# Optimization experiments

Hardware: AMD Instinct MI355X
Metric: run time of the kernel (lower is better)

The kernel has to match this reference:

```python
import jax, jax.numpy as jnp
import numpy as np

# Multi-res hash grid config (tiny-cuda-nn defaults matching input_ch=32 = 16 levels * 2 feats)
L = 16            # n_levels
F = 2             # n_features_per_level
T = 2 ** 19       # hashmap size per level
BASE_RES = 16
FINEST_RES = 512
_b = np.exp((np.log(FINEST_RES) - np.log(BASE_RES)) / (L - 1))
RES = np.floor(BASE_RES * (_b ** np.arange(L))).astype(np.float32)  # (L,)
PRIMES = jnp.array([1, 2654435761, 805459861], dtype=jnp.uint32)
# 8 binary corner offsets of a voxel
CORNERS = jnp.array([[(i >> d) & 1 for d in range(3)] for i in range(8)], dtype=jnp.uint32)  # (8,3)


def hash_encode(x, tables):
    """x: (N,3) in [0,1]; tables: (L, T, F). Returns (N, L*F)."""
    res = jnp.asarray(RES)                              # (L,)
    xs = x[None, :, :] * res[:, None, None]             # (L,N,3) scaled coords
    x0f = jnp.floor(xs)
    frac = xs - x0f                                     # (L,N,3)
    x0 = x0f.astype(jnp.uint32)
    corners = x0[:, :, None, :] + CORNERS[None, None]   # (L,N,8,3) uint32
    # spatial hash: xor of coord*prime, wraparound uint32 mul
    h = (corners[..., 0] * PRIMES[0]) ^ (corners[..., 1] * PRIMES[1]) ^ (corners[..., 2] * PRIMES[2])
    idx = (h % jnp.uint32(T)).astype(jnp.int32)         # (L,N,8)
    gidx = idx + (jnp.arange(L, dtype=jnp.int32) * T)[:, None, None]
    feats = tables.reshape(L * T, F)[gidx]              # (L,N,8,F) gather
    # trilinear weights per corner
    w = jnp.prod(jnp.where(CORNERS[None, None] == 1, frac[:, :, None, :], 1.0 - frac[:, :, None, :]), axis=-1)  # (L,N,8)
    out = jnp.einsum('lnc,lncf->lnf', w, feats)         # (L,N,F)
    return out.transpose(1, 0, 2).reshape(x.shape[0], L * F)


def setup_inputs() -> dict:
    key = jax.random.key(0)
    ks = jax.random.split(key, 16)
    N = 1048576
    W = 128
    pos_flat = jax.random.uniform(ks[0], (N, 3), dtype=jnp.float32)  # world pts in unit cube
    bbox_min = jnp.zeros((3,), dtype=jnp.float32)
    bbox_max = jnp.ones((3,), dtype=jnp.float32)
    tables = jax.random.uniform(ks[1], (L, T, F), dtype=jnp.float32, minval=-1e-4, maxval=1e-4)
    def lin(k, fan_in, fan_out):
        s = 1.0 / np.sqrt(fan_in)
        return jax.random.uniform(k, (fan_in, fan_out), dtype=jnp.float32, minval=-s, maxval=s)
    return {
        'pos_flat': pos_flat, 'bbox_min': bbox_min, 'bbox_max': bbox_max, 'tables': tables,
        'W0': lin(ks[2], L * F, W), 'b0': jnp.zeros((W,), jnp.float32),
        'W1': lin(ks[3], W, W), 'b1': jnp.zeros((W,), jnp.float32),
        'W2': lin(ks[4], W, W), 'b2': jnp.zeros((W,), jnp.float32),
        'W3': lin(ks[5], W, W), 'b3': jnp.zeros((W,), jnp.float32),
        'Wout': lin(ks[6], W, 4), 'bout': jnp.zeros((4,), jnp.float32),
    }


def reference(pos_flat, bbox_min, bbox_max, tables, W0, b0, W1, b1, W2, b2, W3, b3, Wout, bout):
    # normalize into canonical bbox [0,1]^3
    x = (pos_flat - bbox_min) / (bbox_max - bbox_min)
    h = hash_encode(x, tables)                # (N, 32)
    h = jax.nn.relu(h @ W0 + b0)
    h = jax.nn.relu(h @ W1 + b1)
    h = jax.nn.relu(h @ W2 + b2)
    h = jax.nn.relu(h @ W3 + b3)
    raws = h @ Wout + bout                    # (N, 4) rgb + density
    return raws
```

## Files before the change

kernel.cpp:

```cpp
#include <hip/hip_runtime.h>

typedef _Float16 half8 __attribute__((ext_vector_type(8)));
typedef _Float16 half4 __attribute__((ext_vector_type(4)));
typedef _Float16 half2 __attribute__((ext_vector_type(2)));
typedef float    f32x4 __attribute__((ext_vector_type(4)));
typedef float    f32x2 __attribute__((ext_vector_type(2)));
typedef unsigned u32x2 __attribute__((ext_vector_type(2)));
typedef unsigned u32x4 __attribute__((ext_vector_type(4)));

#define TMASK ((1u << 19) - 1u)
#define HSTRIDE 136
constexpr float SCALE = 65536.0f;
constexpr float INV_SCALE = 1.0f / 65536.0f;

__device__ __constant__ unsigned SC_TAB[8]   = {18, 22, 27, 34, 42, 52, 66, 82};
__device__ __constant__ unsigned SX4_TAB[8]  = {5, 6, 7, 9, 11, 13, 17, 21};
__device__ __constant__ unsigned DOFF16_TAB[8] = {0, 1620, 4524, 9627, 20031, 39435, 74587, 148639};
#define DSLOT_TOTAL 289843u

__global__ void prep_kernel(const float* __restrict__ W0, const float* __restrict__ W1,
                            const float* __restrict__ W2, const float* __restrict__ W3,
                            const float* __restrict__ Wm,
                            const float* __restrict__ b0, const float* __restrict__ b1,
                            const float* __restrict__ b2, const float* __restrict__ b3,
                            const float* __restrict__ bm,
                            _Float16* __restrict__ wsW, float* __restrict__ wsB,
                            const float* __restrict__ tabSrc, _Float16* __restrict__ tabF,
                            int tabBlocks)
{
    if ((int)blockIdx.x < tabBlocks) {
        size_t i = (size_t)blockIdx.x * 256 + threadIdx.x;
        f32x4 v = ((const f32x4*)tabSrc)[i];
        half4 o;
        o[0] = (_Float16)(v.x * SCALE);
        o[1] = (_Float16)(v.y * SCALE);
        o[2] = (_Float16)(v.z * SCALE);
        o[3] = (_Float16)(v.w * SCALE);
        ((half4*)tabF)[i] = o;
        return;
    }
    int gid = ((int)blockIdx.x - tabBlocks) * 256 + threadIdx.x;
    if (gid < 6912) {
        int tile = gid >> 6, lane = gid & 63;
        const float* W; int K, N, toff;
        if (tile < 8)        { W = W0; K = 32;  N = 128; toff = 0;   }
        else if (tile < 40)  { W = W1; K = 128; N = 128; toff = 8;   }
        else if (tile < 72)  { W = W2; K = 128; N = 128; toff = 40;  }
        else if (tile < 104) { W = W3; K = 128; N = 128; toff = 72;  }
        else                 { W = Wm; K = 128; N = 4;   toff = 104; }
        int tt = tile - toff;
        int KT = K >> 5;
        int nt = tt / KT, kt = tt - nt * KT;
        int n = nt * 16 + (lane & 15);
        int kbase = kt * 32 + (lane >> 4) * 8;
        half8 v;
        #pragma unroll
        for (int j = 0; j < 8; j++) {
            int k = kbase + j;
            float w = (n < N) ? W[k * N + n] : 0.0f;
            v[j] = (_Float16)w;
        }
        *(half8*)(wsW + (size_t)gid * 8) = v;
    } else if (gid < 6912 + 528) {
        int i = gid - 6912;
        float v;
        if (i < 512) {
            int layer = i >> 7, n = i & 127;
            const float* b = (layer == 0) ? b0 : (layer == 1) ? b1 : (layer == 2) ? b2 : b3;
            v = b[n] * SCALE;
        } else {
            int n = i - 512;
            v = (n < 4) ? bm[n] * SCALE : 0.0f;
        }
        wsB[i] = v;
    }
}

__global__ void dense_build(const float* __restrict__ tables, unsigned* __restrict__ dense)
{
    unsigned e = blockIdx.x * 256 + threadIdx.x;
    if (e >= DSLOT_TOTAL * 4u) return;
    unsigned slot = e >> 2, j = e & 3u;
    int l = 0;
    #pragma unroll
    for (int i = 1; i < 8; i++) l += (slot >= DOFF16_TAB[i]) ? 1 : 0;
    unsigned local = slot - DOFF16_TAB[l];
    unsigned s = SC_TAB[l], sx4 = SX4_TAB[l];
    unsigned plane = sx4 * s;
    unsigned z = local / plane;
    unsigned rem = local - z * plane;
    unsigned y = rem / sx4;
    unsigned xs = rem - y * sx4;
    unsigned x = xs * 4u + j;
    unsigned h = (x ^ (y * 2654435761u) ^ (z * 805459861u)) & TMASK;
    const float* src = tables + ((size_t)l * 524288u + h) * 2;
    half2 o; o[0] = (_Float16)(src[0] * SCALE); o[1] = (_Float16)(src[1] * SCALE);
    union { half2 h2; unsigned u; } cv; cv.h2 = o;
    dense[e] = cv.u;
}

__global__ __launch_bounds__(256, 4) void encode_kernel(
    const float* __restrict__ pos, const float* __restrict__ bmn, const float* __restrict__ bmx,
    const _Float16* __restrict__ tabFine, const u32x4* __restrict__ dense16,
    _Float16* __restrict__ feat, int npts)
{
    const int lvl0 = (int)(blockIdx.x & 7);
    const int t = (int)threadIdx.x;
    const long p0 = (long)(blockIdx.x >> 3) * 512 + t;
    const float bx = bmn[0], by = bmn[1], bz = bmn[2];
    const float dxr = bmx[0] - bx, dyr = bmx[1] - by, dzr = bmx[2] - bz;
    constexpr float RESL[16] = {16.f, 20.f, 25.f, 32.f, 40.f, 50.f, 64.f, 80.f,
                                101.f, 128.f, 161.f, 203.f, 256.f, 322.f, 406.f, 512.f};
    const int l1 = lvl0 + 8;
    const _Float16* tblB = tabFine + ((size_t)lvl0 << 20);
    const float resF = RESL[l1], resC = RESL[lvl0];
    const unsigned s   = SC_TAB[lvl0];
    const unsigned sx4 = SX4_TAB[lvl0];
    const unsigned plane = sx4 * s;
    const u32x4* dptr = dense16 + DOFF16_TAB[lvl0];

    unsigned fSlot[2][4], fOdd[2][4], cBase[2][4];
    unsigned peM[2], kC[2];
    bool oddF[2], nx3[2];
    float fF[2][3], fC[2][3];

    #pragma unroll
    for (int pt = 0; pt < 2; pt++) {
        const long p = p0 + pt * 256;
        const float nx = (pos[p * 3 + 0] - bx) / dxr;
        const float ny = (pos[p * 3 + 1] - by) / dyr;
        const float nz = (pos[p * 3 + 2] - bz) / dzr;
        {
            float xs = nx * resF, ys = ny * resF, zs = nz * resF;
            float fx = floorf(xs), fy = floorf(ys), fz = floorf(zs);
            unsigned xi = (unsigned)fx, yi = (unsigned)fy, zi = (unsigned)fz;
            fF[pt][0] = xs - fx; fF[pt][1] = ys - fy; fF[pt][2] = zs - fz;
            unsigned hy0 = yi * 2654435761u, hy1 = (yi + 1u) * 2654435761u;
            unsigned hz0 = zi * 805459861u,  hz1 = (zi + 1u) * 805459861u;
            unsigned hyz[4] = {hy0 ^ hz0, hy1 ^ hz0, hy0 ^ hz1, hy1 ^ hz1};
            unsigned e = (xi + 1u) & ~1u, o = xi | 1u;
            oddF[pt] = (xi & 1u) != 0u;
            unsigned m = 0;
            #pragma unroll
            for (int g = 0; g < 4; g++) {
                unsigned ie = (e ^ hyz[g]) & TMASK;
                fSlot[pt][g] = ie & ~1u;
                m |= (ie & 1u) << g;
                fOdd[pt][g] = (o ^ hyz[g]) & TMASK;
            }
            peM[pt] = m;
        }
        {
            float xs = nx * resC, ys = ny * resC, zs = nz * resC;
            float fx = floorf(xs), fy = floorf(ys), fz = floorf(zs);
            unsigned xi = (unsigned)fx, yi = (unsigned)fy, zi = (unsigned)fz;
            fC[pt][0] = xs - fx; fC[pt][1] = ys - fy; fC[pt][2] = zs - fz;
            unsigned b00 = (xi >> 2) + sx4 * yi + plane * zi;
            cBase[pt][0] = b00;
            cBase[pt][1] = b00 + sx4;
            cBase[pt][2] = b00 + plane;
            cBase[pt][3] = b00 + plane + sx4;
            kC[pt] = xi & 3u;
            nx3[pt] = (kC[pt] == 3u);
        }
    }

    u32x2 fS[2][4]; u32x4 cS[2][4]; unsigned fO[2][4], cN[2][4];
    #pragma unroll
    for (int pt = 0; pt < 2; pt++) {
        #pragma unroll
        for (int g = 0; g < 4; g++)
            fS[pt][g] = *(const u32x2*)(tblB + (size_t)fSlot[pt][g] * 2);
        #pragma unroll
        for (int g = 0; g < 4; g++)
            cS[pt][g] = dptr[cBase[pt][g]];
        if (oddF[pt]) {
            #pragma unroll
            for (int g = 0; g < 4; g++)
                fO[pt][g] = *(const unsigned*)(tblB + (size_t)fOdd[pt][g] * 2);
        }
        if (nx3[pt]) {
            #pragma unroll
            for (int g = 0; g < 4; g++)
                cN[pt][g] = *(const unsigned*)(dptr + cBase[pt][g] + 1);
        }
    }

    #pragma unroll
    for (int pt = 0; pt < 2; pt++) {
        const long p = p0 + pt * 256;
        {
            float tx = fF[pt][0], ty = fF[pt][1], tz = fF[pt][2];
            float wyz[4] = {(1.0f - ty) * (1.0f - tz), ty * (1.0f - tz),
                            (1.0f - ty) * tz,          ty * tz};
            float b0 = 0.0f, b1 = 0.0f;
            #pragma unroll
            for (int g = 0; g < 4; g++) {
                union { unsigned u; half2 h; } lo, hi, ov;
                lo.u = fS[pt][g][0]; hi.u = fS[pt][g][1];
                bool pe = ((peM[pt] >> g) & 1u) != 0u;
                half2 fe  = pe ? hi.h : lo.h;
                half2 fe1 = pe ? lo.h : hi.h;
                ov.u = oddF[pt] ? fO[pt][g] : 0u;
                half2 fx0 = oddF[pt] ? ov.h : fe;
                half2 fx1 = oddF[pt] ? fe : fe1;
                float w0 = wyz[g] * (1.0f - tx), w1 = wyz[g] * tx;
                b0 += w0 * (float)fx0[0] + w1 * (float)fx1[0];
                b1 += w0 * (float)fx0[1] + w1 * (float)fx1[1];
            }
            half2 ov2; ov2[0] = (_Float16)b0; ov2[1] = (_Float16)b1;
            union { half2 h; unsigned u; } cv; cv.h = ov2;
            __builtin_nontemporal_store(cv.u, (unsigned*)(feat + ((size_t)l1 * npts + p) * 2));
        }
        {
            float tx = fC[pt][0], ty = fC[pt][1], tz = fC[pt][2];
            float wyz[4] = {(1.0f - ty) * (1.0f - tz), ty * (1.0f - tz),
                            (1.0f - ty) * tz,          ty * tz};
            unsigned k = kC[pt];
            unsigned kp1 = (k < 3u) ? (k + 1u) : 0u;
            float a0 = 0.0f, a1 = 0.0f;
            #pragma unroll
            for (int g = 0; g < 4; g++) {
                union { unsigned u; half2 h; } u0, u1;
                u0.u = cS[pt][g][k];
                u1.u = nx3[pt] ? cN[pt][g] : cS[pt][g][kp1];
                float w0 = wyz[g] * (1.0f - tx), w1 = wyz[g] * tx;
                a0 += w0 * (float)u0.h[0] + w1 * (float)u1.h[0];
                a1 += w0 * (float)u0.h[1] + w1 * (float)u1.h[1];
            }
            half2 ov2; ov2[0] = (_Float16)a0; ov2[1] = (_Float16)a1;
            union { half2 h; unsigned u; } cv; cv.h = ov2;
            __builtin_nontemporal_store(cv.u, (unsigned*)(feat + ((size_t)lvl0 * npts + p) * 2));
        }
    }
}

#define ELANE 68

template<int KT, int TOFF>
__device__ __forceinline__ void layer_fwd4(half8 b[4][4], const half8* __restrict__ wf,
                                           const float* __restrict__ wsB, int li,
                                           unsigned* __restrict__ eb, int lane, int quad,
                                           unsigned srcA, unsigned srcB, int mtbase)
{
    unsigned* wptr = eb + lane * ELANE;
    #pragma unroll
    for (int mt = 0; mt < 8; mt++) {
        f32x4 bias = *(const f32x4*)&wsB[li * 128 + mt * 16 + quad * 4];
        half8 w[KT];
        #pragma unroll
        for (int kt = 0; kt < KT; kt++)
            w[kt] = wf[(size_t)(TOFF + mt * KT + kt) * 64 + lane];
        f32x4 acc[4] = {bias, bias, bias, bias};
        #pragma unroll
        for (int nt = 0; nt < 4; nt++)
            #pragma unroll
            for (int kt = 0; kt < KT; kt++)
                acc[nt] = __builtin_amdgcn_mfma_f32_16x16x32_f16(w[kt], b[nt][kt], acc[nt], 0, 0, 0);
        #pragma unroll
        for (int np = 0; np < 2; np++) {
            union { _Float16 h[8]; u32x4 v; } pk;
            #pragma unroll
            for (int r = 0; r < 4; r++) {
                pk.h[r]     = (_Float16)fmaxf(acc[2 * np][r],     0.0f);
                pk.h[4 + r] = (_Float16)fmaxf(acc[2 * np + 1][r], 0.0f);
            }
            *(u32x4*)(wptr + mt * 8 + np * 4) = pk.v;
        }
    }
    #pragma unroll
    for (int ktp = 0; ktp < 4; ktp++) {
        int mt = 2 * ktp + mtbase;
        u32x4 rA0 = *(const u32x4*)(eb + srcA * ELANE + mt * 8);
        u32x4 rA1 = *(const u32x4*)(eb + srcA * ELANE + mt * 8 + 4);
        u32x4 rB0 = *(const u32x4*)(eb + srcB * ELANE + mt * 8);
        u32x4 rB1 = *(const u32x4*)(eb + srcB * ELANE + mt * 8 + 4);
        union { u32x4 v; half8 h; } c0, c1, c2, c3;
        c0.v = (u32x4){rA0[0], rA0[1], rB0[0], rB0[1]};
        c1.v = (u32x4){rA0[2], rA0[3], rB0[2], rB0[3]};
        c2.v = (u32x4){rA1[0], rA1[1], rB1[0], rB1[1]};
        c3.v = (u32x4){rA1[2], rA1[3], rB1[2], rB1[3]};
        b[0][ktp] = c0.h;
        b[1][ktp] = c1.h;
        b[2][ktp] = c2.h;
        b[3][ktp] = c3.h;
    }
}

__global__ __launch_bounds__(256) void mlp_kernel(
    const unsigned* __restrict__ feat32, const half8* __restrict__ wf,
    const float* __restrict__ wsB, float* __restrict__ out, int npts)
{
    __shared__ __align__(16) unsigned ebuf[4 * 64 * ELANE];
    const int t = threadIdx.x;
    const int lane = t & 63, wv = t >> 6;
    const int col = lane & 15, quad = lane >> 4;
    const long base = (long)blockIdx.x * 256 + wv * 64;
    unsigned* eb = ebuf + wv * (64 * ELANE);
    const int q1 = 2 * (quad & 1);
    const unsigned srcA = (unsigned)(col + 16 * q1);
    const unsigned srcB = (unsigned)(col + 16 * (q1 + 1));
    const int mtbase = quad >> 1;

    half8 b[4][4];
    #pragma unroll
    for (int nt = 0; nt < 4; nt++) {
        const long pt = base + nt * 16 + col;
        union { unsigned u4[4]; half8 v; } cv;
        #pragma unroll
        for (int jj = 0; jj < 4; jj++)
            cv.u4[jj] = feat32[(size_t)(quad * 4 + jj) * npts + pt];
        b[nt][0] = cv.v;
    }

    layer_fwd4<1, 0 >(b, wf, wsB, 0, eb, lane, quad, srcA, srcB, mtbase);
    layer_fwd4<4, 8 >(b, wf, wsB, 1, eb, lane, quad, srcA, srcB, mtbase);
    layer_fwd4<4, 40>(b, wf, wsB, 2, eb, lane, quad, srcA, srcB, mtbase);
    layer_fwd4<4, 72>(b, wf, wsB, 3, eb, lane, quad, srcA, srcB, mtbase);

    f32x4 biaso = *(const f32x4*)&wsB[512 + quad * 4];
    f32x4 acco[4] = {biaso, biaso, biaso, biaso};
    #pragma unroll
    for (int kt = 0; kt < 4; kt++) {
        half8 w = wf[(size_t)(104 + kt) * 64 + lane];
        #pragma unroll
        for (int nt = 0; nt < 4; nt++)
            acco[nt] = __builtin_amdgcn_mfma_f32_16x16x32_f16(w, b[nt][kt], acco[nt], 0, 0, 0);
    }
    if (quad == 0) {
        #pragma unroll
        for (int nt = 0; nt < 4; nt++) {
            f32x4 v;
            #pragma unroll
            for (int r = 0; r < 4; r++) v[r] = acco[nt][r] * INV_SCALE;
            *(f32x4*)(out + (base + nt * 16 + col) * 4) = v;
        }
    }
}

template<int KT, int TOFF, bool RELU>
__device__ __forceinline__ void mlp_layer(_Float16* h, const half8* __restrict__ wf,
                                          const float* __restrict__ wsB, int layerIdx,
                                          int m0, int lane)
{
    const int col = lane & 15, quad = lane >> 4;
    const int sw = (col & 3) << 3;
    half8 a[2][KT];
    #pragma unroll
    for (int mt = 0; mt < 2; mt++)
        #pragma unroll
        for (int kt = 0; kt < KT; kt++)
            a[mt][kt] = *(const half8*)&h[(m0 + mt * 16 + col) * HSTRIDE + ((kt * 32 + quad * 8) ^ sw)];
    f32x4 acc[2][8];
    #pragma unroll
    for (int nt = 0; nt < 8; nt++) {
        float bv = wsB[layerIdx * 128 + nt * 16 + col];
        acc[0][nt] = (f32x4){bv, bv, bv, bv};
        acc[1][nt] = (f32x4){bv, bv, bv, bv};
    }
    #pragma unroll
    for (int nt = 0; nt < 8; nt++) {
        half8 b[KT];
        #pragma unroll
        for (int kt = 0; kt < KT; kt++)
            b[kt] = wf[(size_t)(TOFF + nt * KT + kt) * 64 + lane];
        #pragma unroll
        for (int mt = 0; mt < 2; mt++)
            #pragma unroll
            for (int kt = 0; kt < KT; kt++)
                acc[mt][nt] = __builtin_amdgcn_mfma_f32_16x16x32_f16(a[mt][kt], b[kt], acc[mt][nt], 0, 0, 0);
    }
    #pragma unroll
    for (int mt = 0; mt < 2; mt++)
        #pragma unroll
        for (int nt = 0; nt < 8; nt++) {
            f32x4 v = acc[mt][nt];
            #pragma unroll
            for (int r = 0; r < 4; r++) {
                float x = v[r];
                if (RELU) x = fmaxf(x, 0.0f);
                h[(m0 + mt * 16 + quad * 4 + r) * HSTRIDE + ((nt * 16 + col) ^ (r << 3))] = (_Float16)x;
            }
        }
}

__global__ __launch_bounds__(256, 2) void fused_kernel(
    const float* __restrict__ pos, const float* __restrict__ bmn, const float* __restrict__ bmx,
    const float* __restrict__ tables, const half8* __restrict__ wf, const float* __restrict__ wsB,
    float* __restrict__ out)
{
    __shared__ _Float16 hbuf[128 * HSTRIDE];
    __shared__ float outstage[512];
    const int t = threadIdx.x;
    const long base = (long)blockIdx.x * 128;
    {
        const int p = t >> 1, hh = t & 1;
        const long gp = base + p;
        const float b0x = bmn[0], b0y = bmn[1], b0z = bmn[2];
        const float nx = (pos[gp * 3 + 0] - b0x) / (bmx[0] - b0x);
        const float ny = (pos[gp * 3 + 1] - b0y) / (bmx[1] - b0y);
        const float nz = (pos[gp * 3 + 2] - b0z) / (bmx[2] - b0z);
        constexpr float RLO[8] = {16.f, 20.f, 25.f, 32.f, 40.f, 50.f, 64.f, 80.f};
        constexpr float RHI[8] = {101.f, 128.f, 161.f, 203.f, 256.f, 322.f, 406.f, 512.f};
        half8 fa, fb;
        #pragma unroll
        for (int li = 0; li < 8; li++) {
            const float res = hh ? RHI[li] : RLO[li];
            const float* tbl = tables + ((size_t)(hh * 8 + li) << 20);
            float xs = nx * res, ys = ny * res, zs = nz * res;
            float fx = floorf(xs), fy = floorf(ys), fz = floorf(zs);
            unsigned xi = (unsigned)fx, yi = (unsigned)fy, zi = (unsigned)fz;
            float tx = xs - fx, ty = ys - fy, tz = zs - fz;
            unsigned hx[2] = {xi, xi + 1u};
            unsigned hy[2] = {yi * 2654435761u, (yi + 1u) * 2654435761u};
            unsigned hz[2] = {zi * 805459861u, (zi + 1u) * 805459861u};
            float wx[2] = {1.0f - tx, tx}, wy[2] = {1.0f - ty, ty}, wz[2] = {1.0f - tz, tz};
            float a0 = 0.0f, a1 = 0.0f;
            #pragma unroll
            for (int c = 0; c < 8; c++) {
                unsigned hsh = hx[c & 1] ^ hy[(c >> 1) & 1] ^ hz[c >> 2];
                unsigned idx = hsh & TMASK;
                f32x2 f = *(const f32x2*)(tbl + (size_t)idx * 2);
                float w = wx[c & 1] * wy[(c >> 1) & 1] * wz[c >> 2];
                a0 += w * f.x;
                a1 += w * f.y;
            }
            if (li < 4) { fa[2 * li]       = (_Float16)(a0 * SCALE); fa[2 * li + 1]       = (_Float16)(a1 * SCALE); }
            else        { fb[2 * (li - 4)] = (_Float16)(a0 * SCALE); fb[2 * (li - 4) + 1] = (_Float16)(a1 * SCALE); }
        }
        const int sw = (p & 3) << 3;
        *(half8*)&hbuf[p * HSTRIDE + ((hh * 16) ^ sw)]       = fa;
        *(half8*)&hbuf[p * HSTRIDE + (((hh * 16) + 8) ^ sw)] = fb;
    }
    __syncthreads();
    {
        const int lane = t & 63;
        const int m0 = (t >> 6) * 32;
        mlp_layer<1, 0,   true>(hbuf, wf, wsB, 0, m0, lane);
        mlp_layer<4, 8,   true>(hbuf, wf, wsB, 1, m0, lane);
        mlp_layer<4, 40,  true>(hbuf, wf, wsB, 2, m0, lane);
        mlp_layer<4, 72,  true>(hbuf, wf, wsB, 3, m0, lane);
        const int col = lane & 15, quad = lane >> 4;
        const int sw = (col & 3) << 3;
        half8 a[2][4];
        #pragma unroll
        for (int mt = 0; mt < 2; mt++)
            #pragma unroll
            for (int kt = 0; kt < 4; kt++)
                a[mt][kt] = *(const half8*)&hbuf[(m0 + mt * 16 + col) * HSTRIDE + ((kt * 32 + quad * 8) ^ sw)];
        float bv = wsB[512 + col];
        f32x4 acc[2] = {(f32x4){bv, bv, bv, bv}, (f32x4){bv, bv, bv, bv}};
        #pragma unroll
        for (int kt = 0; kt < 4; kt++) {
            half8 bfr = wf[(size_t)(104 + kt) * 64 + lane];
            #pragma unroll
            for (int mt = 0; mt < 2; mt++)
                acc[mt] = __builtin_amdgcn_mfma_f32_16x16x32_f16(a[mt][kt], bfr, acc[mt], 0, 0, 0);
        }
        if (col < 4) {
            #pragma unroll
            for (int mt = 0; mt < 2; mt++)
                #pragma unroll
                for (int r = 0; r < 4; r++)
                    outstage[(m0 + mt * 16 + quad * 4 + r) * 4 + col] = acc[mt][r] * INV_SCALE;
        }
    }
    __syncthreads();
    if (t < 128) {
        f32x4 v = ((const f32x4*)outstage)[t];
        *(f32x4*)(out + (base + t) * 4) = v;
    }
}

extern "C" void kernel_launch(void* const* d_in, const int* in_sizes, int n_in,
                              void* d_out, int out_size, void* d_ws, size_t ws_size,
                              hipStream_t stream) {
    const float* pos    = (const float*)d_in[0];
    const float* bmn    = (const float*)d_in[1];
    const float* bmx    = (const float*)d_in[2];
    const float* tables = (const float*)d_in[3];
    const float* W0 = (const float*)d_in[4];
    const float* b0 = (const float*)d_in[5];
    const float* W1 = (const float*)d_in[6];
    const float* b1 = (const float*)d_in[7];
    const float* W2 = (const float*)d_in[8];
    const float* b2 = (const float*)d_in[9];
    const float* W3 = (const float*)d_in[10];
    const float* b3 = (const float*)d_in[11];
    const float* Wm = (const float*)d_in[12];
    const float* bm = (const float*)d_in[13];

    const int N = in_sizes[0] / 3;
    const size_t featBytes    = (size_t)N * 16 * 4;
    const size_t tabFineBytes = (size_t)8 * 524288 * 2 * 2;
    const size_t denseBytes   = ((size_t)DSLOT_TOTAL * 16 + 255) & ~(size_t)255;
    const size_t need = featBytes + tabFineBytes + denseBytes + 110592 + 2112;

    if (ws_size >= need && (N % 512) == 0) {
        _Float16* feat  = (_Float16*)d_ws;
        _Float16* tabF  = (_Float16*)((char*)d_ws + featBytes);
        unsigned* dense = (unsigned*)((char*)d_ws + featBytes + tabFineBytes);
        _Float16* wsW   = (_Float16*)((char*)d_ws + featBytes + tabFineBytes + denseBytes);
        float*    wsB   = (float*)((char*)d_ws + featBytes + tabFineBytes + denseBytes + 110592);
        prep_kernel<<<8192 + 30, 256, 0, stream>>>(W0, W1, W2, W3, Wm, b0, b1, b2, b3, bm,
                                                   wsW, wsB, tables + (size_t)8 * 524288 * 2,
                                                   tabF, 8192);
        dense_build<<<(DSLOT_TOTAL * 4 + 255) / 256, 256, 0, stream>>>(tables, dense);
        encode_kernel<<<(N / 512) * 8, 256, 0, stream>>>(pos, bmn, bmx, tabF,
                                                         (const u32x4*)dense, feat, N);
        mlp_kernel<<<N / 256, 256, 0, stream>>>((const unsigned*)feat, (const half8*)wsW,
                                                wsB, (float*)d_out, N);
    } else {
        _Float16* wsW = (_Float16*)d_ws;
        float*    wsB = (float*)((char*)d_ws + 110592);
        prep_kernel<<<30, 256, 0, stream>>>(W0, W1, W2, W3, Wm, b0, b1, b2, b3, bm,
                                            wsW, wsB, tables, (_Float16*)nullptr, 0);
        fused_kernel<<<N / 128, 256, 0, stream>>>(pos, bmn, bmx, tables,
                                                  (const half8*)wsW, wsB, (float*)d_out);
    }
}
```

Measured before the change: 617.6 us.

## Software-pipeline encode kernel over eight points per thread with double-buffered loads

The encode kernel now handles eight points per thread instead of two. It uses a two-slot rotation: the gathers for the next point are issued before the current point's loaded values are consumed. The aim is to keep more hash-table gathers in flight per thread and to amortize per-block setup, hiding gather latency. The grid shrinks by four times and the fast path now requires N divisible by 2048. Register pressure may rise and fewer blocks may be in flight.

```diff
diff --git a/kernel.cpp b/kernel.cpp
--- a/kernel.cpp
+++ b/kernel.cpp
@@ -99,6 +99,16 @@
     dense[e] = cv.u;
 }
 
+struct PtState {
+    unsigned fSlot[4], fOdd[4], cBase[4];
+    unsigned peM, kC;
+    bool oddF, nx3;
+    float fF[3], fC[3];
+};
+struct PtLoads {
+    u32x2 fS[4]; u32x4 cS[4]; unsigned fO[4], cN[4];
+};
+
 __global__ __launch_bounds__(256, 4) void encode_kernel(
     const float* __restrict__ pos, const float* __restrict__ bmn, const float* __restrict__ bmx,
     const _Float16* __restrict__ tabFine, const u32x4* __restrict__ dense16,
@@ -106,7 +116,7 @@
 {
     const int lvl0 = (int)(blockIdx.x & 7);
     const int t = (int)threadIdx.x;
-    const long p0 = (long)(blockIdx.x >> 3) * 512 + t;
+    const long pb = (long)(blockIdx.x >> 3) * 2048 + t;
     const float bx = bmn[0], by = bmn[1], bz = bmn[2];
     const float dxr = bmx[0] - bx, dyr = bmx[1] - by, dzr = bmx[2] - bz;
     constexpr float RESL[16] = {16.f, 20.f, 25.f, 32.f, 40.f, 50.f, 64.f, 80.f,
@@ -114,19 +124,11 @@
     const int l1 = lvl0 + 8;
     const _Float16* tblB = tabFine + ((size_t)lvl0 << 20);
     const float resF = RESL[l1], resC = RESL[lvl0];
-    const unsigned s   = SC_TAB[lvl0];
     const unsigned sx4 = SX4_TAB[lvl0];
-    const unsigned plane = sx4 * s;
+    const unsigned plane = sx4 * SC_TAB[lvl0];
     const u32x4* dptr = dense16 + DOFF16_TAB[lvl0];
 
-    unsigned fSlot[2][4], fOdd[2][4], cBase[2][4];
-    unsigned peM[2], kC[2];
-    bool oddF[2], nx3[2];
-    float fF[2][3], fC[2][3];
-
-    #pragma unroll
-    for (int pt = 0; pt < 2; pt++) {
-        const long p = p0 + pt * 256;
+    auto computePt = [&](long p, PtState& S) {
         const float nx = (pos[p * 3 + 0] - bx) / dxr;
         const float ny = (pos[p * 3 + 1] - by) / dyr;
         const float nz = (pos[p * 3 + 2] - bz) / dzr;
@@ -134,76 +136,72 @@
             float xs = nx * resF, ys = ny * resF, zs = nz * resF;
             float fx = floorf(xs), fy = floorf(ys), fz = floorf(zs);
             unsigned xi = (unsigned)fx, yi = (unsigned)fy, zi = (unsigned)fz;
-            fF[pt][0] = xs - fx; fF[pt][1] = ys - fy; fF[pt][2] = zs - fz;
+            S.fF[0] = xs - fx; S.fF[1] = ys - fy; S.fF[2] = zs - fz;
             unsigned hy0 = yi * 2654435761u, hy1 = (yi + 1u) * 2654435761u;
             unsigned hz0 = zi * 805459861u,  hz1 = (zi + 1u) * 805459861u;
             unsigned hyz[4] = {hy0 ^ hz0, hy1 ^ hz0, hy0 ^ hz1, hy1 ^ hz1};
             unsigned e = (xi + 1u) & ~1u, o = xi | 1u;
-            oddF[pt] = (xi & 1u) != 0u;
+            S.oddF = (xi & 1u) != 0u;
             unsigned m = 0;
             #pragma unroll
             for (int g = 0; g < 4; g++) {
                 unsigned ie = (e ^ hyz[g]) & TMASK;
-                fSlot[pt][g] = ie & ~1u;
+                S.fSlot[g] = ie & ~1u;
                 m |= (ie & 1u) << g;
-                fOdd[pt][g] = (o ^ hyz[g]) & TMASK;
+                S.fOdd[g] = (o ^ hyz[g]) & TMASK;
             }
-            peM[pt] = m;
+            S.peM = m;
         }
         {
             float xs = nx * resC, ys = ny * resC, zs = nz * resC;
             float fx = floorf(xs), fy = floorf(ys), fz = floorf(zs);
             unsigned xi = (unsigned)fx, yi = (unsigned)fy, zi = (unsigned)fz;
-            fC[pt][0] = xs - fx; fC[pt][1] = ys - fy; fC[pt][2] = zs - fz;
+            S.fC[0] = xs - fx; S.fC[1] = ys - fy; S.fC[2] = zs - fz;
             unsigned b00 = (xi >> 2) + sx4 * yi + plane * zi;
-            cBase[pt][0] = b00;
-            cBase[pt][1] = b00 + sx4;
-            cBase[pt][2] = b00 + plane;
-            cBase[pt][3] = b00 + plane + sx4;
-            kC[pt] = xi & 3u;
-            nx3[pt] = (kC[pt] == 3u);
-        }
-    }
-
-    u32x2 fS[2][4]; u32x4 cS[2][4]; unsigned fO[2][4], cN[2][4];
-    #pragma unroll
-    for (int pt = 0; pt < 2; pt++) {
+            S.cBase[0] = b00;
+            S.cBase[1] = b00 + sx4;
+            S.cBase[2] = b00 + plane;
+            S.cBase[3] = b00 + plane + sx4;
+            S.kC = xi & 3u;
+            S.nx3 = (S.kC == 3u);
+        }
+    };
+
+    auto issuePt = [&](const PtState& S, PtLoads& L) {
         #pragma unroll
         for (int g = 0; g < 4; g++)
-            fS[pt][g] = *(const u32x2*)(tblB + (size_t)fSlot[pt][g] * 2);
+            L.fS[g] = *(const u32x2*)(tblB + (size_t)S.fSlot[g] * 2);
         #pragma unroll
         for (int g = 0; g < 4; g++)
-            cS[pt][g] = dptr[cBase[pt][g]];
-        if (oddF[pt]) {
+            L.cS[g] = dptr[S.cBase[g]];
+        if (S.oddF) {
             #pragma unroll
             for (int g = 0; g < 4; g++)
-                fO[pt][g] = *(const unsigned*)(tblB + (size_t)fOdd[pt][g] * 2);
-        }
-        if (nx3[pt]) {
+                L.fO[g] = *(const unsigned*)(tblB + (size_t)S.fOdd[g] * 2);
+        }
+        if (S.nx3) {
             #pragma unroll
             for (int g = 0; g < 4; g++)
-                cN[pt][g] = *(const unsigned*)(dptr + cBase[pt][g] + 1);
-        }
-    }
-
-    #pragma unroll
-    for (int pt = 0; pt < 2; pt++) {
-        const long p = p0 + pt * 256;
+                L.cN[g] = *(const unsigned*)(dptr + S.cBase[g] + 1);
+        }
+    };
+
+    auto consumePt = [&](const PtState& S, const PtLoads& L, long p) {
         {
-            float tx = fF[pt][0], ty = fF[pt][1], tz = fF[pt][2];
+            float tx = S.fF[0], ty = S.fF[1], tz = S.fF[2];
             float wyz[4] = {(1.0f - ty) * (1.0f - tz), ty * (1.0f - tz),
                             (1.0f - ty) * tz,          ty * tz};
             float b0 = 0.0f, b1 = 0.0f;
             #pragma unroll
             for (int g = 0; g < 4; g++) {
                 union { unsigned u; half2 h; } lo, hi, ov;
-                lo.u = fS[pt][g][0]; hi.u = fS[pt][g][1];
-                bool pe = ((peM[pt] >> g) & 1u) != 0u;
+                lo.u = L.fS[g][0]; hi.u = L.fS[g][1];
+                bool pe = ((S.peM >> g) & 1u) != 0u;
                 half2 fe  = pe ? hi.h : lo.h;
                 half2 fe1 = pe ? lo.h : hi.h;
-                ov.u = oddF[pt] ? fO[pt][g] : 0u;
-                half2 fx0 = oddF[pt] ? ov.h : fe;
-                half2 fx1 = oddF[pt] ? fe : fe1;
+                ov.u = S.oddF ? L.fO[g] : 0u;
+                half2 fx0 = S.oddF ? ov.h : fe;
+                half2 fx1 = S.oddF ? fe : fe1;
                 float w0 = wyz[g] * (1.0f - tx), w1 = wyz[g] * tx;
                 b0 += w0 * (float)fx0[0] + w1 * (float)fx1[0];
                 b1 += w0 * (float)fx0[1] + w1 * (float)fx1[1];
@@ -213,17 +211,17 @@
             __builtin_nontemporal_store(cv.u, (unsigned*)(feat + ((size_t)l1 * npts + p) * 2));
         }
         {
-            float tx = fC[pt][0], ty = fC[pt][1], tz = fC[pt][2];
+            float tx = S.fC[0], ty = S.fC[1], tz = S.fC[2];
             float wyz[4] = {(1.0f - ty) * (1.0f - tz), ty * (1.0f - tz),
                             (1.0f - ty) * tz,          ty * tz};
-            unsigned k = kC[pt];
+            unsigned k = S.kC;
             unsigned kp1 = (k < 3u) ? (k + 1u) : 0u;
             float a0 = 0.0f, a1 = 0.0f;
             #pragma unroll
             for (int g = 0; g < 4; g++) {
                 union { unsigned u; half2 h; } u0, u1;
-                u0.u = cS[pt][g][k];
-                u1.u = nx3[pt] ? cN[pt][g] : cS[pt][g][kp1];
+                u0.u = L.cS[g][k];
+                u1.u = S.nx3 ? L.cN[g] : L.cS[g][kp1];
                 float w0 = wyz[g] * (1.0f - tx), w1 = wyz[g] * tx;
                 a0 += w0 * (float)u0.h[0] + w1 * (float)u1.h[0];
                 a1 += w0 * (float)u0.h[1] + w1 * (float)u1.h[1];
@@ -232,7 +230,23 @@
             union { half2 h; unsigned u; } cv; cv.h = ov2;
             __builtin_nontemporal_store(cv.u, (unsigned*)(feat + ((size_t)lvl0 * npts + p) * 2));
         }
-    }
+    };
+
+    PtState sA, sB; PtLoads lA, lB;
+    computePt(pb + 0 * 256, sA); issuePt(sA, lA);
+    computePt(pb + 1 * 256, sB); issuePt(sB, lB);
+    #pragma unroll
+    for (int k = 0; k < 6; k++) {
+        if ((k & 1) == 0) {
+            consumePt(sA, lA, pb + (long)k * 256);
+            computePt(pb + (long)(k + 2) * 256, sA); issuePt(sA, lA);
+        } else {
+            consumePt(sB, lB, pb + (long)k * 256);
+            computePt(pb + (long)(k + 2) * 256, sB); issuePt(sB, lB);
+        }
+    }
+    consumePt(sA, lA, pb + 6 * 256);
+    consumePt(sB, lB, pb + 7 * 256);
 }
 
 #define ELANE 68
@@ -496,7 +510,7 @@
     const size_t denseBytes   = ((size_t)DSLOT_TOTAL * 16 + 255) & ~(size_t)255;
     const size_t need = featBytes + tabFineBytes + denseBytes + 110592 + 2112;
 
-    if (ws_size >= need && (N % 512) == 0) {
+    if (ws_size >= need && (N % 2048) == 0) {
         _Float16* feat  = (_Float16*)d_ws;
         _Float16* tabF  = (_Float16*)((char*)d_ws + featBytes);
         unsigned* dense = (unsigned*)((char*)d_ws + featBytes + tabFineBytes);
@@ -506,8 +520,8 @@
                                                    wsW, wsB, tables + (size_t)8 * 524288 * 2,
                                                    tabF, 8192);
         dense_build<<<(DSLOT_TOTAL * 4 + 255) / 256, 256, 0, stream>>>(tables, dense);
-        encode_kernel<<<(N / 512) * 8, 256, 0, stream>>>(pos, bmn, bmx, tabF,
-                                                         (const u32x4*)dense, feat, N);
+        encode_kernel<<<(N / 2048) * 8, 256, 0, stream>>>(pos, bmn, bmx, tabF,
+                                                          (const u32x4*)dense, feat, N);
         mlp_kernel<<<N / 256, 256, 0, stream>>>((const unsigned*)feat, (const half8*)wsW,
                                                 wsB, (float*)d_out, N);
     } else {
```

Result: no change. 617.7 us (+0.0%).
